# Kernel optimization log

Measured on AMD Instinct MI355X. Metric: run time of the kernel, lower is better.

The kernel has to match this reference:

```python
import jax, jax.numpy as jnp
import numpy as np

D_MODEL = 1024
NUM_HEADS = 16
HEAD_DIM = D_MODEL // NUM_HEADS
B, S = 4, 2048


def _xavier(key, shape, gain=0.1):
    fan_in, fan_out = shape[1], shape[0]
    a = gain * np.sqrt(6.0 / (fan_in + fan_out))
    return jax.random.uniform(key, shape, jnp.float32, -a, a)


def setup_inputs() -> dict:
    key = jax.random.key(0)
    ks = jax.random.split(key, 11)
    inp = {
        "q": jax.random.normal(ks[0], (B, S, D_MODEL), jnp.float32),
        "k": jax.random.normal(ks[1], (B, S, D_MODEL), jnp.float32),
        "v": jax.random.normal(ks[2], (B, S, D_MODEL), jnp.float32),
        # nn.Linear weights are [out, in]; y = x @ W.T + b
        "Wq": _xavier(ks[3], (D_MODEL, D_MODEL)),
        "bq": jnp.zeros((D_MODEL,), jnp.float32),
        "Wk": _xavier(ks[4], (D_MODEL, D_MODEL)),
        "bk": jnp.zeros((D_MODEL,), jnp.float32),
        "Wv": _xavier(ks[5], (D_MODEL, D_MODEL)),
        "bv": jnp.zeros((D_MODEL,), jnp.float32),
        "Wo": _xavier(ks[6], (D_MODEL, D_MODEL)),
        "bo": jnp.zeros((D_MODEL,), jnp.float32),
    }
    return inp


def reference(q, k, v, Wq, bq, Wk, bk, Wv, bv, Wo, bo):
    b = q.shape[0]
    qh = (q @ Wq.T + bq).reshape(b, -1, NUM_HEADS, HEAD_DIM).transpose(0, 2, 1, 3)
    kh = (k @ Wk.T + bk).reshape(b, -1, NUM_HEADS, HEAD_DIM).transpose(0, 2, 1, 3)
    vh = (v @ Wv.T + bv).reshape(b, -1, NUM_HEADS, HEAD_DIM).transpose(0, 2, 1, 3)
    # NOTE: original (buggy) module scales by sqrt(d_model), not sqrt(head_dim)
    scale = 1.0 / jnp.sqrt(jnp.float32(D_MODEL))
    scores = jnp.einsum('bhqd,bhkd->bhqk', qh, kh) * scale  # [B,H,S,S]
    attn = jax.nn.softmax(scores, axis=-1)
    out = jnp.einsum('bhqk,bhkd->bhqd', attn, vh)
    out = out.transpose(0, 2, 1, 3).reshape(b, -1, D_MODEL)
    return out @ Wo.T + bo
```

## Files before the change

kernel.cpp:

```cpp
#include <hip/hip_runtime.h>

typedef unsigned short u16;
typedef short bf16x8 __attribute__((ext_vector_type(8)));
typedef float f32x4 __attribute__((ext_vector_type(4)));
typedef u16 u16x8 __attribute__((ext_vector_type(8)));

__device__ __forceinline__ u16 f2bf(float f) {
  unsigned u = __float_as_uint(f);
  u = u + 0x7fffu + ((u >> 16) & 1u);
  return (u16)(u >> 16);
}

__device__ __forceinline__ float fexp2(float x) {
#if __has_builtin(__builtin_amdgcn_exp2f)
  return __builtin_amdgcn_exp2f(x);
#else
  return exp2f(x);
#endif
}

#define GLD16(ldsp, gp)                                                         \
  __builtin_amdgcn_global_load_lds(                                             \
      (__attribute__((address_space(1))) void*)(void*)(gp),                     \
      (__attribute__((address_space(3))) void*)(ldsp), 16, 0, 0)

#define CVTPK(dst, lo, hi)                                                      \
  asm("v_cvt_pk_bf16_f32 %0, %1, %2" : "=v"(dst) : "v"(lo), "v"(hi))
#define PACK8(dst, a0, a1, a2, a3, a4, a5, a6, a7)                              \
  do {                                                                          \
    union { unsigned u_[4]; bf16x8 v_; } c_;                                    \
    CVTPK(c_.u_[0], a0, a1); CVTPK(c_.u_[1], a2, a3);                           \
    CVTPK(c_.u_[2], a4, a5); CVTPK(c_.u_[3], a6, a7);                           \
    dst = c_.v_;                                                                \
  } while (0)

__global__ __launch_bounds__(256) void pack_w4(const float* __restrict__ w0,
                                               const float* __restrict__ w1,
                                               const float* __restrict__ w2,
                                               const float* __restrict__ w3,
                                               u16* __restrict__ out) {
  int i = blockIdx.x * 256 + threadIdx.x;
  int which = i >> 17;
  const float* src = which == 0 ? w0 : which == 1 ? w1 : which == 2 ? w2 : w3;
  int j = i & 131071;
  const float4* p = (const float4*)src + (size_t)j * 2;
  float4 a = p[0], b = p[1];
  u16x8 r;
  r[0] = f2bf(a.x); r[1] = f2bf(a.y); r[2] = f2bf(a.z); r[3] = f2bf(a.w);
  r[4] = f2bf(b.x); r[5] = f2bf(b.y); r[6] = f2bf(b.z); r[7] = f2bf(b.w);
  *(u16x8*)(out + (size_t)i * 8) = r;
}

__global__ __launch_bounds__(256, 4)
void gemm_qkv(const float* __restrict__ qi, const float* __restrict__ ki,
              const float* __restrict__ vi, const u16* __restrict__ wbf,
              const float* __restrict__ bq, const float* __restrict__ bk,
              const float* __restrict__ bv, u16* __restrict__ qo,
              u16* __restrict__ ko, u16* __restrict__ vo) {
  constexpr int K = 1024;
  __shared__ __align__(16) u16 As[128 * 64];
  __shared__ __align__(16) u16 Bs[128 * 64];
  const int z = blockIdx.z;
  const float* Af = z == 0 ? qi : z == 1 ? ki : vi;
  const u16* Bw = wbf + ((size_t)z << 20);
  const float* bias = z == 0 ? bq : z == 1 ? bk : bv;

  const int t = threadIdx.x;
  const int w = t >> 6, l = t & 63;
  const int lr = l & 15, lg = l >> 4;
  const int flat = blockIdx.x | (blockIdx.y << 3);
  const int swz = ((flat & 7) << 6) | (flat >> 3);
  const int row0 = (swz >> 3) * 128, col0 = (swz & 7) * 128;
  const int wm = (w >> 1) * 64, wn = (w & 1) * 64;

  f32x4 acc[4][4] = {};

  const int ar = t >> 3;
  const int xw = ((t & 7) ^ (ar & 7)) * 16;
  const float* gA = Af + (size_t)(row0 + ar) * K + (t & 7) * 8;
  const u16* gB = Bw + (size_t)(col0 + ar) * K + (((t & 7) ^ (ar & 7)) * 8);
  u16* lB = &Bs[w * 512];

  float4 a0[4], a1[4];
#pragma unroll
  for (int j = 0; j < 4; ++j) {
    const float* p = gA + (size_t)j * 32 * K;
    a0[j] = *(const float4*)p;
    a1[j] = *(const float4*)(p + 4);
  }

  for (int kt = 0; kt < 16; ++kt) {
#pragma unroll
    for (int j = 0; j < 4; ++j)
      GLD16(lB + j * 2048, gB + (size_t)j * 32 * K + kt * 64);
#pragma unroll
    for (int j = 0; j < 4; ++j) {
      bf16x8 c;
      PACK8(c, a0[j].x, a0[j].y, a0[j].z, a0[j].w, a1[j].x, a1[j].y, a1[j].z, a1[j].w);
      *(bf16x8*)((char*)As + (ar + j * 32) * 128 + xw) = c;
    }
    __syncthreads();
    if (kt < 15) {
#pragma unroll
      for (int j = 0; j < 4; ++j) {
        const float* p = gA + (size_t)j * 32 * K + (kt + 1) * 64;
        a0[j] = *(const float4*)p;
        a1[j] = *(const float4*)(p + 4);
      }
    }
#pragma unroll
    for (int kh2 = 0; kh2 < 2; ++kh2) {
      bf16x8 aF[4], bF[4];
      const int bc = (kh2 * 64 + lg * 16) ^ ((lr & 7) * 16);
#pragma unroll
      for (int mi = 0; mi < 4; ++mi)
        aF[mi] = *(const bf16x8*)((const char*)As + (wm + mi * 16 + lr) * 128 + bc);
#pragma unroll
      for (int ni = 0; ni < 4; ++ni)
        bF[ni] = *(const bf16x8*)((const char*)Bs + (wn + ni * 16 + lr) * 128 + bc);
#pragma unroll
      for (int mi = 0; mi < 4; ++mi)
#pragma unroll
        for (int ni = 0; ni < 4; ++ni)
          acc[mi][ni] = __builtin_amdgcn_mfma_f32_16x16x32_bf16(aF[mi], bF[ni],
                                                                acc[mi][ni], 0, 0, 0);
    }
    __syncthreads();
  }

#pragma unroll
  for (int mi = 0; mi < 4; ++mi) {
#pragma unroll
    for (int ni = 0; ni < 4; ++ni) {
      const int n = col0 + wn + ni * 16 + lr;
      const float bvv = bias[n];
#pragma unroll
      for (int r = 0; r < 4; ++r) {
        const int m = row0 + wm + mi * 16 + lg * 4 + r;
        const float vv = acc[mi][ni][r] + bvv;
        const int bI = m >> 11, s = m & 2047, h = n >> 6, d = n & 63;
        if (z == 0) {
          qo[((size_t)((bI << 4) + h) * 2048 + s) * 64 + d] = f2bf(vv * 0.045084223f);
        } else if (z == 1) {
          ko[((size_t)((bI << 4) + h) * 2048 + s) * 64 + d] = f2bf(vv);
        } else {
          int bh = (bI << 4) + h, tile = s >> 6, kp = s & 63;
          int kM = kp >> 5, k5 = kp & 31;
          int kpp = kM * 32 + ((k5 >> 2) & 3) * 8 + (k5 >> 4) * 4 + (k5 & 3);
          int chunk = (kpp >> 3) ^ (d & 7);
          vo[((size_t)bh << 17) + tile * 4096 + d * 64 + chunk * 8 + (kpp & 7)] = f2bf(vv);
        }
      }
    }
  }
}

__global__ __launch_bounds__(256, 3)
void gemm_out(const u16* __restrict__ A, const u16* __restrict__ B,
              const float* __restrict__ bias, float* __restrict__ outp) {
  constexpr int K = 1024;
  __shared__ __align__(16) u16 As[128 * 64];
  __shared__ __align__(16) u16 Bs[128 * 64];
  const int t = threadIdx.x;
  const int w = t >> 6;
  const int l = t & 63;
  const int lr = l & 15, lg = l >> 4;
  const int flat = blockIdx.x | (blockIdx.y << 3);
  const int swz = ((flat & 7) << 6) | (flat >> 3);
  const int row0 = (swz >> 3) * 128, col0 = (swz & 7) * 128;
  const int wm = (w >> 1) * 64, wn = (w & 1) * 64;

  f32x4 acc[4][4] = {};

  const int srow = t >> 3;
  const int scol = ((t & 7) ^ (srow & 7)) * 8;
  const u16* gA = A + (size_t)(row0 + srow) * K + scol;
  const u16* gB = B + (size_t)(col0 + srow) * K + scol;
  u16* lA = &As[w * 512];
  u16* lB = &Bs[w * 512];

  for (int k0 = 0; k0 < K; k0 += 64) {
#pragma unroll
    for (int j = 0; j < 4; ++j) {
      GLD16(lA + j * 2048, gA + (size_t)j * 32 * K + k0);
      GLD16(lB + j * 2048, gB + (size_t)j * 32 * K + k0);
    }
    __syncthreads();
#pragma unroll
    for (int kh2 = 0; kh2 < 2; ++kh2) {
      bf16x8 aF[4], bF[4];
      const int bc = (kh2 * 64 + lg * 16) ^ ((lr & 7) * 16);
#pragma unroll
      for (int mi = 0; mi < 4; ++mi)
        aF[mi] = *(const bf16x8*)((const char*)As + (wm + mi * 16 + lr) * 128 + bc);
#pragma unroll
      for (int ni = 0; ni < 4; ++ni)
        bF[ni] = *(const bf16x8*)((const char*)Bs + (wn + ni * 16 + lr) * 128 + bc);
#pragma unroll
      for (int mi = 0; mi < 4; ++mi)
#pragma unroll
        for (int ni = 0; ni < 4; ++ni)
          acc[mi][ni] = __builtin_amdgcn_mfma_f32_16x16x32_bf16(aF[mi], bF[ni],
                                                                acc[mi][ni], 0, 0, 0);
    }
    __syncthreads();
  }

#pragma unroll
  for (int mi = 0; mi < 4; ++mi)
#pragma unroll
    for (int ni = 0; ni < 4; ++ni) {
      const int n = col0 + wn + ni * 16 + lr;
      const float bv = bias[n];
#pragma unroll
      for (int r = 0; r < 4; ++r) {
        const int m = row0 + wm + mi * 16 + lg * 4 + r;
        outp[(size_t)m * 1024 + n] = acc[mi][ni][r] + bv;
      }
    }
}

__global__ __launch_bounds__(256, 4)
void attn_fwd(const u16* __restrict__ qh, const u16* __restrict__ kh,
              const u16* __restrict__ vp, u16* __restrict__ aout) {
  __shared__ __align__(16) u16 Ks[2][4096];
  __shared__ __align__(16) u16 Vl[2][4096];
  const int t = threadIdx.x;
  const int w = t >> 6, l = t & 63;
  const int lr = l & 15, lg = l >> 4;
  const int flat = blockIdx.x | (blockIdx.y << 4);
  const int swz = ((flat & 7) << 7) | (flat >> 3);
  const int qb = swz & 15, bh = swz >> 4;
  const int q0 = qb * 128 + w * 32;

  bf16x8 qf[2][2];
#pragma unroll
  for (int qi = 0; qi < 2; ++qi) {
    const u16* qp = qh + ((size_t)bh * 2048 + q0 + qi * 16 + lr) * 64 + lg * 8;
    qf[qi][0] = *(const bf16x8*)qp;
    qf[qi][1] = *(const bf16x8*)(qp + 32);
  }

  f32x4 o0[4] = {}, o1[4] = {};
  float lsum0 = 0.f, lsum1 = 0.f;

  const int krow = t >> 3, kseg = t & 7;
  const u16* gK = kh + ((size_t)bh * 2048 + krow) * 64 + ((kseg ^ (krow & 7)) * 8);
  const u16* gV = vp + ((size_t)bh << 17) + t * 8;

  const int xo0 = (lg * 16) ^ ((lr & 7) * 16);
  const int xo1 = xo0 ^ 64;

  {
    u16* kd = &Ks[0][0] + w * 512;
    u16* vd = &Vl[0][0] + w * 512;
    GLD16(kd, gK); GLD16(kd + 2048, gK + 2048);
    GLD16(vd, gV); GLD16(vd + 2048, gV + 2048);
    gK += 4096; gV += 4096;
  }
  __syncthreads();

  for (int tix = 0; tix < 32; ++tix) {
    const int cur = tix & 1;
    if (tix < 31) {
      u16* kd = &Ks[cur ^ 1][0] + w * 512;
      u16* vd = &Vl[cur ^ 1][0] + w * 512;
      GLD16(kd, gK); GLD16(kd + 2048, gK + 2048);
      GLD16(vd, gV); GLD16(vd + 2048, gV + 2048);
      gK += 4096; gV += 4096;
    }
    const char* kb = (const char*)&Ks[cur][0];
    f32x4 s0[4], s1[4];
    __builtin_amdgcn_s_setprio(1);
#pragma unroll
    for (int cq = 0; cq < 4; ++cq) {
      const char* rowp = kb + (cq * 16 + lr) * 128;
      bf16x8 kf0 = *(const bf16x8*)(rowp + xo0);
      bf16x8 kf1 = *(const bf16x8*)(rowp + xo1);
      f32x4 a = {}, b2 = {};
      a  = __builtin_amdgcn_mfma_f32_16x16x32_bf16(kf0, qf[0][0], a, 0, 0, 0);
      a  = __builtin_amdgcn_mfma_f32_16x16x32_bf16(kf1, qf[0][1], a, 0, 0, 0);
      b2 = __builtin_amdgcn_mfma_f32_16x16x32_bf16(kf0, qf[1][0], b2, 0, 0, 0);
      b2 = __builtin_amdgcn_mfma_f32_16x16x32_bf16(kf1, qf[1][1], b2, 0, 0, 0);
      s0[cq] = a; s1[cq] = b2;
    }
    __builtin_amdgcn_s_setprio(0);
    float p0[16], p1[16];
#pragma unroll
    for (int cq = 0; cq < 4; ++cq)
#pragma unroll
      for (int r = 0; r < 4; ++r) {
        p0[cq * 4 + r] = fexp2(s0[cq][r]);
        p1[cq * 4 + r] = fexp2(s1[cq][r]);
      }
    float a0 = 0.f, a1 = 0.f;
#pragma unroll
    for (int i = 0; i < 16; ++i) { a0 += p0[i]; a1 += p1[i]; }
    lsum0 += a0; lsum1 += a1;
    bf16x8 pA0, pA1, pB0, pB1;
    PACK8(pA0, p0[0], p0[1], p0[2], p0[3], p0[4], p0[5], p0[6], p0[7]);
    PACK8(pA1, p0[8], p0[9], p0[10], p0[11], p0[12], p0[13], p0[14], p0[15]);
    PACK8(pB0, p1[0], p1[1], p1[2], p1[3], p1[4], p1[5], p1[6], p1[7]);
    PACK8(pB1, p1[8], p1[9], p1[10], p1[11], p1[12], p1[13], p1[14], p1[15]);
    __builtin_amdgcn_s_setprio(1);
    const char* vbb = (const char*)&Vl[cur][0];
#pragma unroll
    for (int dc = 0; dc < 4; ++dc) {
      const char* rp = vbb + (dc * 16 + lr) * 128;
      bf16x8 vA = *(const bf16x8*)(rp + xo0);
      bf16x8 vB = *(const bf16x8*)(rp + xo1);
      o0[dc] = __builtin_amdgcn_mfma_f32_16x16x32_bf16(pA0, vA, o0[dc], 0, 0, 0);
      o0[dc] = __builtin_amdgcn_mfma_f32_16x16x32_bf16(pA1, vB, o0[dc], 0, 0, 0);
      o1[dc] = __builtin_amdgcn_mfma_f32_16x16x32_bf16(pB0, vA, o1[dc], 0, 0, 0);
      o1[dc] = __builtin_amdgcn_mfma_f32_16x16x32_bf16(pB1, vB, o1[dc], 0, 0, 0);
    }
    __builtin_amdgcn_s_setprio(0);
    __syncthreads();
  }

  float sA = lsum0; sA += __shfl_xor(sA, 16); sA += __shfl_xor(sA, 32);
  float sB = lsum1; sB += __shfl_xor(sB, 16); sB += __shfl_xor(sB, 32);
  const int b = bh >> 4, h = bh & 15;
#pragma unroll
  for (int r = 0; r < 4; ++r) {
    const float dA = 1.f / __shfl(sA, lg * 4 + r);
    const float dB = 1.f / __shfl(sB, lg * 4 + r);
    const size_t rowA = (size_t)b * 2048 + q0 + lg * 4 + r;
#pragma unroll
    for (int dc = 0; dc < 4; ++dc) {
      aout[rowA * 1024 + h * 64 + dc * 16 + lr] = f2bf(o0[dc][r] * dA);
      aout[(rowA + 16) * 1024 + h * 64 + dc * 16 + lr] = f2bf(o1[dc][r] * dB);
    }
  }
}

extern "C" void kernel_launch(void* const* d_in, const int* in_sizes, int n_in,
                              void* d_out, int out_size, void* d_ws, size_t ws_size,
                              hipStream_t stream) {
  const float* q  = (const float*)d_in[0];
  const float* k  = (const float*)d_in[1];
  const float* v  = (const float*)d_in[2];
  const float* Wq = (const float*)d_in[3];
  const float* bq = (const float*)d_in[4];
  const float* Wk = (const float*)d_in[5];
  const float* bk = (const float*)d_in[6];
  const float* Wv = (const float*)d_in[7];
  const float* bv = (const float*)d_in[8];
  const float* Wo = (const float*)d_in[9];
  const float* bo = (const float*)d_in[10];

  char* ws = (char*)d_ws;
  u16* wbf  = (u16*)(ws);
  u16* aout = (u16*)(ws + (8ull << 20));
  u16* qhB  = (u16*)(ws + (24ull << 20));
  u16* khB  = (u16*)(ws + (40ull << 20));
  u16* vtB  = (u16*)(ws + (56ull << 20));

  pack_w4<<<2048, 256, 0, stream>>>(Wq, Wk, Wv, Wo, wbf);
  gemm_qkv<<<dim3(8, 64, 3), 256, 0, stream>>>(q, k, v, wbf, bq, bk, bv,
                                               qhB, khB, vtB);
  attn_fwd<<<dim3(16, 64), 256, 0, stream>>>(qhB, khB, vtB, aout);
  gemm_out<<<dim3(8, 64), 256, 0, stream>>>(aout, wbf + (3u << 20), bo,
                                            (float*)d_out);

  (void)in_sizes; (void)n_in; (void)out_size; (void)ws_size;
}
```

Before: 169.5 us.

## Double per-wave query rows in attention to reuse K/V tiles across more queries

Each attention workgroup now processes 256 query rows (64 per wave, four 16-row sub-tiles) instead of 128, halving the grid and the number of times each K/V block is streamed into LDS. Each K and V fragment read from LDS feeds four MFMA groups instead of two, cutting LDS and global traffic per FLOP. In exchange, register pressure doubles (launch bounds lowered to 2 blocks per CU), so occupancy and latency hiding drop, and the 512-block grid may underfill the GPU.

Result: no change. 172.6 us (+1.9%).

```diff
diff --git a/kernel.cpp b/kernel.cpp
--- a/kernel.cpp
+++ b/kernel.cpp
@@ -220,7 +220,7 @@
     }
 }
 
-__global__ __launch_bounds__(256, 4)
+__global__ __launch_bounds__(256, 2)
 void attn_fwd(const u16* __restrict__ qh, const u16* __restrict__ kh,
               const u16* __restrict__ vp, u16* __restrict__ aout) {
   __shared__ __align__(16) u16 Ks[2][4096];
@@ -228,21 +228,21 @@
   const int t = threadIdx.x;
   const int w = t >> 6, l = t & 63;
   const int lr = l & 15, lg = l >> 4;
-  const int flat = blockIdx.x | (blockIdx.y << 4);
-  const int swz = ((flat & 7) << 7) | (flat >> 3);
-  const int qb = swz & 15, bh = swz >> 4;
-  const int q0 = qb * 128 + w * 32;
-
-  bf16x8 qf[2][2];
-#pragma unroll
-  for (int qi = 0; qi < 2; ++qi) {
-    const u16* qp = qh + ((size_t)bh * 2048 + q0 + qi * 16 + lr) * 64 + lg * 8;
-    qf[qi][0] = *(const bf16x8*)qp;
-    qf[qi][1] = *(const bf16x8*)(qp + 32);
-  }
-
-  f32x4 o0[4] = {}, o1[4] = {};
-  float lsum0 = 0.f, lsum1 = 0.f;
+  const int flat = blockIdx.x | (blockIdx.y << 3);
+  const int swz = ((flat & 7) << 6) | (flat >> 3);
+  const int qb = swz & 7, bh = swz >> 3;
+  const int q0 = qb * 256 + w * 64;
+
+  bf16x8 qf[4][2];
+#pragma unroll
+  for (int s = 0; s < 4; ++s) {
+    const u16* qp = qh + ((size_t)bh * 2048 + q0 + s * 16 + lr) * 64 + lg * 8;
+    qf[s][0] = *(const bf16x8*)qp;
+    qf[s][1] = *(const bf16x8*)(qp + 32);
+  }
+
+  f32x4 o[4][4] = {};
+  float lsum[4] = {0.f, 0.f, 0.f, 0.f};
 
   const int krow = t >> 3, kseg = t & 7;
   const u16* gK = kh + ((size_t)bh * 2048 + krow) * 64 + ((kseg ^ (krow & 7)) * 8);
@@ -270,66 +270,72 @@
       gK += 4096; gV += 4096;
     }
     const char* kb = (const char*)&Ks[cur][0];
-    f32x4 s0[4], s1[4];
+    f32x4 sq[4][4];
     __builtin_amdgcn_s_setprio(1);
 #pragma unroll
     for (int cq = 0; cq < 4; ++cq) {
       const char* rowp = kb + (cq * 16 + lr) * 128;
       bf16x8 kf0 = *(const bf16x8*)(rowp + xo0);
       bf16x8 kf1 = *(const bf16x8*)(rowp + xo1);
-      f32x4 a = {}, b2 = {};
-      a  = __builtin_amdgcn_mfma_f32_16x16x32_bf16(kf0, qf[0][0], a, 0, 0, 0);
-      a  = __builtin_amdgcn_mfma_f32_16x16x32_bf16(kf1, qf[0][1], a, 0, 0, 0);
-      b2 = __builtin_amdgcn_mfma_f32_16x16x32_bf16(kf0, qf[1][0], b2, 0, 0, 0);
-      b2 = __builtin_amdgcn_mfma_f32_16x16x32_bf16(kf1, qf[1][1], b2, 0, 0, 0);
-      s0[cq] = a; s1[cq] = b2;
+#pragma unroll
+      for (int s = 0; s < 4; ++s) {
+        f32x4 a = {};
+        a = __builtin_amdgcn_mfma_f32_16x16x32_bf16(kf0, qf[s][0], a, 0, 0, 0);
+        a = __builtin_amdgcn_mfma_f32_16x16x32_bf16(kf1, qf[s][1], a, 0, 0, 0);
+        sq[s][cq] = a;
+      }
     }
     __builtin_amdgcn_s_setprio(0);
-    float p0[16], p1[16];
-#pragma unroll
-    for (int cq = 0; cq < 4; ++cq)
-#pragma unroll
-      for (int r = 0; r < 4; ++r) {
-        p0[cq * 4 + r] = fexp2(s0[cq][r]);
-        p1[cq * 4 + r] = fexp2(s1[cq][r]);
-      }
-    float a0 = 0.f, a1 = 0.f;
-#pragma unroll
-    for (int i = 0; i < 16; ++i) { a0 += p0[i]; a1 += p1[i]; }
-    lsum0 += a0; lsum1 += a1;
-    bf16x8 pA0, pA1, pB0, pB1;
-    PACK8(pA0, p0[0], p0[1], p0[2], p0[3], p0[4], p0[5], p0[6], p0[7]);
-    PACK8(pA1, p0[8], p0[9], p0[10], p0[11], p0[12], p0[13], p0[14], p0[15]);
-    PACK8(pB0, p1[0], p1[1], p1[2], p1[3], p1[4], p1[5], p1[6], p1[7]);
-    PACK8(pB1, p1[8], p1[9], p1[10], p1[11], p1[12], p1[13], p1[14], p1[15]);
+#pragma unroll
+    for (int s = 0; s < 4; ++s) {
+      float a0 = 0.f;
+#pragma unroll
+      for (int cq = 0; cq < 4; ++cq)
+#pragma unroll
+        for (int r = 0; r < 4; ++r) {
+          sq[s][cq][r] = fexp2(sq[s][cq][r]);
+          a0 += sq[s][cq][r];
+        }
+      lsum[s] += a0;
+    }
+    bf16x8 pf[4][2];
+#pragma unroll
+    for (int s = 0; s < 4; ++s) {
+      PACK8(pf[s][0], sq[s][0][0], sq[s][0][1], sq[s][0][2], sq[s][0][3],
+                      sq[s][1][0], sq[s][1][1], sq[s][1][2], sq[s][1][3]);
+      PACK8(pf[s][1], sq[s][2][0], sq[s][2][1], sq[s][2][2], sq[s][2][3],
+                      sq[s][3][0], sq[s][3][1], sq[s][3][2], sq[s][3][3]);
+    }
+    const char* vbb = (const char*)&Vl[cur][0];
     __builtin_amdgcn_s_setprio(1);
-    const char* vbb = (const char*)&Vl[cur][0];
 #pragma unroll
     for (int dc = 0; dc < 4; ++dc) {
       const char* rp = vbb + (dc * 16 + lr) * 128;
       bf16x8 vA = *(const bf16x8*)(rp + xo0);
       bf16x8 vB = *(const bf16x8*)(rp + xo1);
-      o0[dc] = __builtin_amdgcn_mfma_f32_16x16x32_bf16(pA0, vA, o0[dc], 0, 0, 0);
-      o0[dc] = __builtin_amdgcn_mfma_f32_16x16x32_bf16(pA1, vB, o0[dc], 0, 0, 0);
-      o1[dc] = __builtin_amdgcn_mfma_f32_16x16x32_bf16(pB0, vA, o1[dc], 0, 0, 0);
-      o1[dc] = __builtin_amdgcn_mfma_f32_16x16x32_bf16(pB1, vB, o1[dc], 0, 0, 0);
+#pragma unroll
+      for (int s = 0; s < 4; ++s) {
+        o[s][dc] = __builtin_amdgcn_mfma_f32_16x16x32_bf16(pf[s][0], vA, o[s][dc], 0, 0, 0);
+        o[s][dc] = __builtin_amdgcn_mfma_f32_16x16x32_bf16(pf[s][1], vB, o[s][dc], 0, 0, 0);
+      }
     }
     __builtin_amdgcn_s_setprio(0);
     __syncthreads();
   }
 
-  float sA = lsum0; sA += __shfl_xor(sA, 16); sA += __shfl_xor(sA, 32);
-  float sB = lsum1; sB += __shfl_xor(sB, 16); sB += __shfl_xor(sB, 32);
   const int b = bh >> 4, h = bh & 15;
 #pragma unroll
-  for (int r = 0; r < 4; ++r) {
-    const float dA = 1.f / __shfl(sA, lg * 4 + r);
-    const float dB = 1.f / __shfl(sB, lg * 4 + r);
-    const size_t rowA = (size_t)b * 2048 + q0 + lg * 4 + r;
-#pragma unroll
-    for (int dc = 0; dc < 4; ++dc) {
-      aout[rowA * 1024 + h * 64 + dc * 16 + lr] = f2bf(o0[dc][r] * dA);
-      aout[(rowA + 16) * 1024 + h * 64 + dc * 16 + lr] = f2bf(o1[dc][r] * dB);
+  for (int s = 0; s < 4; ++s) {
+    float sS = lsum[s];
+    sS += __shfl_xor(sS, 16);
+    sS += __shfl_xor(sS, 32);
+#pragma unroll
+    for (int r = 0; r < 4; ++r) {
+      const float d = 1.f / __shfl(sS, lg * 4 + r);
+      const size_t rowA = (size_t)b * 2048 + q0 + s * 16 + lg * 4 + r;
+#pragma unroll
+      for (int dc = 0; dc < 4; ++dc)
+        aout[rowA * 1024 + h * 64 + dc * 16 + lr] = f2bf(o[s][dc][r] * d);
     }
   }
 }
@@ -359,7 +365,7 @@
   pack_w4<<<2048, 256, 0, stream>>>(Wq, Wk, Wv, Wo, wbf);
   gemm_qkv<<<dim3(8, 64, 3), 256, 0, stream>>>(q, k, v, wbf, bq, bk, bv,
                                                qhB, khB, vtB);
-  attn_fwd<<<dim3(16, 64), 256, 0, stream>>>(qhB, khB, vtB, aout);
+  attn_fwd<<<dim3(8, 64), 256, 0, stream>>>(qhB, khB, vtB, aout);
   gemm_out<<<dim3(8, 64), 256, 0, stream>>>(aout, wbf + (3u << 20), bo,
                                             (float*)d_out);
 
```
